# Kernel optimization log

Measured on AMD Instinct MI355X. Metric: run time of the kernel, lower is better.

Reference implementation:

```python
import jax, jax.numpy as jnp
import numpy as np

IN_CH, OUT_CH, HEADS = 256, 128, 4
DIM_HEAD = OUT_CH // HEADS  # 32 (module overrides dim_head = out_ch // heads)
R = 16  # reduce_size
EPS = 1e-5


def _conv3d(x, w, groups=1, pad=0):
    return jax.lax.conv_general_dilated(
        x, w, (1, 1, 1), [(pad, pad)] * 3,
        dimension_numbers=('NCDHW', 'OIDHW', 'NCDHW'),
        feature_group_count=groups)


def _dwsep(x, wd, wp):
    # depthwise 3x3x3 (groups=C) then pointwise 1x1x1, both bias-free
    y = _conv3d(x, wd, groups=x.shape[1], pad=1)
    return _conv3d(y, wp)


def _bn(x, g, b):
    # training-mode BatchNorm3d: biased batch stats over (N, D, H, W)
    m = x.mean(axis=(0, 2, 3, 4), keepdims=True)
    v = x.var(axis=(0, 2, 3, 4), keepdims=True)
    return (x - m) * jax.lax.rsqrt(v + EPS) * g.reshape(1, -1, 1, 1, 1) + b.reshape(1, -1, 1, 1, 1)


def _interp1(x, axis, out_len):
    in_len = x.shape[axis]
    if in_len == out_len:
        return x
    pos = jnp.arange(out_len, dtype=x.dtype) * ((in_len - 1) / (out_len - 1))  # align_corners=True
    lo = jnp.clip(jnp.floor(pos).astype(jnp.int32), 0, in_len - 1)
    hi = jnp.clip(lo + 1, 0, in_len - 1)
    w = pos - lo.astype(x.dtype)
    shp = [1] * x.ndim
    shp[axis] = out_len
    w = w.reshape(shp)
    return jnp.take(x, lo, axis=axis) * (1 - w) + jnp.take(x, hi, axis=axis) * w


def _interp3(x, size):
    for ax, s in zip((2, 3, 4), size):
        x = _interp1(x, ax, s)
    return x


def _rel_index(h, w, d):
    c = np.stack(np.meshgrid(np.arange(h), np.arange(w), np.arange(d), indexing='ij')).reshape(3, -1)
    rel = (c[:, :, None] - c[:, None, :]).transpose(1, 2, 0).astype(np.int64)
    rel[:, :, 0] += h - 1
    rel[:, :, 1] += w - 1
    rel[:, :, 0] *= 2 * h - 1
    idx = rel.sum(-1)
    # faithful to torch: negative indices wrap around the table
    return idx % ((2 * h - 1) * (2 * w - 1) * (2 * d - 1))


def _rel_bias(table, h, w, d, H, W, D, heads):
    idx = _rel_index(h, w, d)
    bias = table[idx.reshape(-1)].reshape(h, w, d, h * w, -1)
    bias = jnp.repeat(bias, H // h, axis=0)
    bias = jnp.repeat(bias, W // w, axis=1)
    bias = jnp.repeat(bias, D // d, axis=2)
    return bias.reshape(H * W * D, h * w * d, heads).transpose(2, 0, 1)[None]  # [1,heads,Nq,Nk]


def setup_inputs() -> dict:
    key = jax.random.key(0)
    ks = jax.random.split(key, 12)
    n = lambda k, s: jax.random.normal(k, s, dtype=jnp.float32)
    return {
        'x1': n(ks[0], (1, IN_CH, 8, 8, 8)),
        'x2': n(ks[1], (1, OUT_CH, 16, 16, 16)),
        'w_ch': n(ks[2], (OUT_CH, IN_CH, 1, 1, 1)) * 0.05,
        'b_ch': jnp.zeros((OUT_CH,), jnp.float32),
        'gamma_l': jnp.ones((IN_CH,), jnp.float32), 'beta_l': jnp.zeros((IN_CH,), jnp.float32),
        'gamma_h': jnp.ones((OUT_CH,), jnp.float32), 'beta_h': jnp.zeros((OUT_CH,), jnp.float32),
        'gamma2': jnp.ones((OUT_CH,), jnp.float32), 'beta2': jnp.zeros((OUT_CH,), jnp.float32),
        'kv_dw': n(ks[3], (IN_CH, 1, 3, 3, 3)) * 0.05,
        'kv_pw': n(ks[4], (2 * OUT_CH, IN_CH, 1, 1, 1)) * 0.05,
        'q_dw': n(ks[5], (OUT_CH, 1, 3, 3, 3)) * 0.05,
        'q_pw': n(ks[6], (OUT_CH, OUT_CH, 1, 1, 1)) * 0.05,
        'out_dw': n(ks[7], (OUT_CH, 1, 3, 3, 3)) * 0.05,
        'out_pw': n(ks[8], (OUT_CH, OUT_CH, 1, 1, 1)) * 0.05,
        'w_mlp': n(ks[9], (OUT_CH, OUT_CH, 1, 1, 1)) * 0.05,
        'rel_table': n(ks[10], ((2 * R - 1) ** 3, HEADS)) * 0.02,
    }


def reference(x1, x2, w_ch, b_ch, gamma_l, beta_l, gamma_h, beta_h, gamma2, beta2,
              kv_dw, kv_pw, q_dw, q_pw, out_dw, out_pw, w_mlp, rel_table):
    B, C, H, W, D = x1.shape
    _, _, HH, WH, DH = x2.shape
    residue = _interp3(_conv3d(x1, w_ch) + b_ch.reshape(1, -1, 1, 1, 1), (HH, WH, DH))
    x1n = _bn(x1, gamma_l, beta_l)
    x2n = _bn(x2, gamma_h, beta_h)
    k, v = jnp.split(_dwsep(x1n, kv_dw, kv_pw), 2, axis=1)
    q = _dwsep(x2n, q_dw, q_pw)
    if H != R:
        k = _interp3(k, (R, R, R))
        v = _interp3(v, (R, R, R))

    def heads_split(t, h, w_, d):
        # channel layout is (dim_head, heads)
        t = t.reshape(B, DIM_HEAD, HEADS, h, w_, d)
        return t.transpose(0, 2, 3, 4, 5, 1).reshape(B, HEADS, h * w_ * d, DIM_HEAD)

    qh = heads_split(q, HH, WH, DH)
    kh = heads_split(k, R, R, R)
    vh = heads_split(v, R, R, R)
    attn = jnp.einsum('bhid,bhjd->bhij', qh, kh)
    attn = attn + _rel_bias(rel_table, R, R, R, HH, WH, DH, HEADS)
    attn = jax.nn.softmax(attn * (DIM_HEAD ** -0.5), axis=-1)  # note: bias is scaled too, as in source
    o = jnp.einsum('bhij,bhjd->bhid', attn, vh)
    o = o.reshape(B, HEADS, HH, WH, DH, DIM_HEAD).transpose(0, 5, 1, 2, 3, 4).reshape(B, OUT_CH, HH, WH, DH)
    o = _dwsep(o, out_dw, out_pw)
    o = o + residue
    res2 = o
    o = jax.nn.relu(_bn(o, gamma2, beta2))
    o = _conv3d(o, w_mlp)
    return o + res2
```

## Files before the change

kernel.cpp:

```cpp
#include <hip/hip_runtime.h>
#include <hip/hip_bf16.h>

using f32x4  = __attribute__((ext_vector_type(4))) float;
using bf16x8 = __attribute__((ext_vector_type(8))) short;
using i32x4  = __attribute__((ext_vector_type(4))) int;

static constexpr float SCALE = 0.17677669529663687f;
static constexpr float L2E   = 1.4426950408889634f;
static constexpr float SL    = SCALE * L2E;

__device__ inline int cvtpk(float lo, float hi) {
  int r;
  asm("v_cvt_pk_bf16_f32 %0,%1,%2" : "=v"(r) : "v"(lo), "v"(hi));
  return r;
}

__device__ inline void bred2(float& s, float& ss) {
  #pragma unroll
  for (int off = 32; off; off >>= 1) {
    s  += __shfl_down(s, off, 64);
    ss += __shfl_down(ss, off, 64);
  }
  __shared__ float as_[4], ass_[4];
  int wid = threadIdx.x >> 6;
  if ((threadIdx.x & 63) == 0) { as_[wid] = s; ass_[wid] = ss; }
  __syncthreads();
  s  = as_[0] + as_[1] + as_[2] + as_[3];
  ss = ass_[0] + ass_[1] + ass_[2] + ass_[3];
}

__global__ __launch_bounds__(256) void bnstat_both_kernel(
    const float* __restrict__ x1, const float* __restrict__ x2,
    const float* __restrict__ gl, const float* __restrict__ bl,
    const float* __restrict__ gh, const float* __restrict__ bh,
    float* __restrict__ ab_l, float* __restrict__ ab_h) {
  int b = blockIdx.x;
  const float* src; const float *gamma, *beta; float* ab; int S, C, c;
  if (b < 256) { c = b;       src = x1 + (size_t)c * 512;  S = 512;  C = 256; gamma = gl; beta = bl; ab = ab_l; }
  else         { c = b - 256; src = x2 + (size_t)c * 4096; S = 4096; C = 128; gamma = gh; beta = bh; ab = ab_h; }
  float s = 0.f, ss = 0.f;
  for (int i = threadIdx.x; i < S; i += 256) { float v = src[i]; s += v; ss = fmaf(v, v, ss); }
  bred2(s, ss);
  if (threadIdx.x == 0) {
    float inv = 1.0f / (float)S;
    float m   = s * inv;
    float var = ss * inv - m * m;
    float a   = gamma[c] * rsqrtf(var + 1e-5f);
    ab[c]     = a;
    ab[C + c] = beta[c] - m * a;
  }
}

template<bool AFF>
__device__ inline void dw_body(
    const float* __restrict__ in, const float* __restrict__ w,
    const float* __restrict__ ab, float* __restrict__ out,
    int n, int nn, int n3, int C, int t) {
  int c = t / n3, s = t - c * n3;
  int z = s / nn, r = s - z * nn, y = r / n, x = r - y * n;
  const float* src = in + (size_t)c * n3;
  const float* wc  = w + c * 27;
  float a = 1.f, b = 0.f;
  if (AFF) { a = ab[c]; b = ab[C + c]; }
  float acc = 0.f;
  #pragma unroll
  for (int kd = 0; kd < 3; kd++) {
    int zz = z + kd - 1;
    if (zz < 0 || zz >= n) continue;
    #pragma unroll
    for (int kh = 0; kh < 3; kh++) {
      int yy = y + kh - 1;
      if (yy < 0 || yy >= n) continue;
      #pragma unroll
      for (int kw = 0; kw < 3; kw++) {
        int xx = x + kw - 1;
        if (xx < 0 || xx >= n) continue;
        float v = src[(zz * n + yy) * n + xx];
        if (AFF) v = fmaf(v, a, b);
        acc = fmaf(v, wc[kd * 9 + kh * 3 + kw], acc);
      }
    }
  }
  out[t] = acc;
}

__global__ __launch_bounds__(256) void stageA_kernel(
    const float* __restrict__ x1, const float* __restrict__ x2,
    const float* __restrict__ w_ch, const float* __restrict__ b_ch,
    const float* __restrict__ kv_dw, const float* __restrict__ q_dw,
    const float* __restrict__ ab_l, const float* __restrict__ ab_h,
    float* __restrict__ res8, float* __restrict__ kvdw, float* __restrict__ qdw) {
  int b = blockIdx.x;
  if (b < 128) {
    int oc0 = (b >> 1) * 2;
    int s   = (b & 1) * 256 + threadIdx.x;
    float a0 = 0.f, a1 = 0.f;
    const float* w0 = w_ch + (size_t)oc0 * 256;
    const float* w1 = w0 + 256;
    #pragma unroll 8
    for (int ic = 0; ic < 256; ic++) {
      float x = x1[(size_t)ic * 512 + s];
      a0 = fmaf(w0[ic], x, a0);
      a1 = fmaf(w1[ic], x, a1);
    }
    res8[(size_t)oc0 * 512 + s]       = a0 + b_ch[oc0];
    res8[(size_t)(oc0 + 1) * 512 + s] = a1 + b_ch[oc0 + 1];
  } else if (b < 640) {
    dw_body<true>(x1, kv_dw, ab_l, kvdw, 8, 64, 512, 256, (b - 128) * 256 + threadIdx.x);
  } else {
    dw_body<true>(x2, q_dw, ab_h, qdw, 16, 256, 4096, 128, (b - 640) * 256 + threadIdx.x);
  }
}

__device__ inline void icoef8(int o, int& lo, int& hi, float& w) {
  float p = (float)o * (7.0f / 15.0f);
  int l = (int)floorf(p);
  if (l > 7) l = 7;
  int h = l + 1 > 7 ? 7 : l + 1;
  w  = p - (float)l;
  lo = l; hi = h;
}

__device__ inline float trilin8(const float* __restrict__ p,
                                int z0, int z1, float wz,
                                int y0, int y1, float wy,
                                int x0, int x1, float wx) {
  float c00 = p[(z0*8+y0)*8+x0]*(1.f-wx) + p[(z0*8+y0)*8+x1]*wx;
  float c01 = p[(z0*8+y1)*8+x0]*(1.f-wx) + p[(z0*8+y1)*8+x1]*wx;
  float c10 = p[(z1*8+y0)*8+x0]*(1.f-wx) + p[(z1*8+y0)*8+x1]*wx;
  float c11 = p[(z1*8+y1)*8+x0]*(1.f-wx) + p[(z1*8+y1)*8+x1]*wx;
  float c0 = c00*(1.f-wy) + c01*wy;
  float c1 = c10*(1.f-wy) + c11*wy;
  return c0*(1.f-wz) + c1*wz;
}

__global__ __launch_bounds__(512) void stageB_kernel(
    const float* __restrict__ kvdw, const float* __restrict__ kv_pw,
    const float* __restrict__ qdw, const float* __restrict__ q_pw,
    const float* __restrict__ res8,
    unsigned short* __restrict__ Kb, unsigned short* __restrict__ Vt,
    unsigned short* __restrict__ Qpk, float* __restrict__ r16) {
  __shared__ float sm[2][512];
  int b = blockIdx.x;
  int tid = threadIdx.x;
  if (b < 128) {
    int kc0 = b * 2;
    int s = tid;
    float a0 = 0.f, a1 = 0.f;
    const float* w0 = kv_pw + (size_t)kc0 * 256;
    const float* w1 = w0 + 256;
    #pragma unroll 8
    for (int ic = 0; ic < 256; ic++) {
      float x = kvdw[(size_t)ic * 512 + s];
      a0 = fmaf(w0[ic], x, a0);
      a1 = fmaf(w1[ic], x, a1);
    }
    sm[0][s] = a0; sm[1][s] = a1;
    __syncthreads();
    #pragma unroll
    for (int r = 0; r < 16; r++) {
      int u  = r * 512 + tid;
      int cl = u >> 12, j = u & 4095;
      int z = j >> 8, y = (j >> 4) & 15, x = j & 15;
      int z0,z1,y0,y1,x0,x1; float wz,wy,wx;
      icoef8(z, z0, z1, wz); icoef8(y, y0, y1, wy); icoef8(x, x0, x1, wx);
      float val = trilin8(sm[cl], z0, z1, wz, y0, y1, wy, x0, x1, wx);
      __hip_bfloat16 bv = __float2bfloat16(val);
      unsigned short us = *reinterpret_cast<unsigned short*>(&bv);
      int kc = kc0 + cl;
      int c  = kc & 127;
      int head = c & 3, dh = c >> 2;
      if (kc < 128) Kb[((size_t)(head << 12) + j) * 32 + dh] = us;
      else          Vt[((size_t)(head * 32) + dh) * 4096 + j] = us;
    }
  } else if (b < 256) {
    int bb   = b - 128;
    int head = bb >> 5;
    int r2   = bb & 31;
    int dh0  = (r2 >> 3) * 8;
    int i    = (r2 & 7) * 512 + tid;
    float acc[8];
    #pragma unroll
    for (int e = 0; e < 8; e++) acc[e] = 0.f;
    #pragma unroll 4
    for (int ic = 0; ic < 128; ic++) {
      float x = qdw[(size_t)ic * 4096 + i];
      #pragma unroll
      for (int e = 0; e < 8; e++)
        acc[e] = fmaf(q_pw[(size_t)((dh0 + e) * 4 + head) * 128 + ic], x, acc[e]);
    }
    i32x4 pk = { cvtpk(acc[0], acc[1]), cvtpk(acc[2], acc[3]),
                 cvtpk(acc[4], acc[5]), cvtpk(acc[6], acc[7]) };
    *reinterpret_cast<i32x4*>(Qpk + ((size_t)(head << 12) + i) * 32 + dh0) = pk;
  } else {
    int t = (b - 256) * 512 + tid;
    int s = t & 4095, c = t >> 12;
    int z = s >> 8, y = (s >> 4) & 15, x = s & 15;
    int z0,z1,y0,y1,x0,x1; float wz,wy,wx;
    icoef8(z, z0, z1, wz); icoef8(y, y0, y1, wy); icoef8(x, x0, x1, wx);
    r16[t] = trilin8(res8 + c * 512, z0, z1, wz, y0, y1, wy, x0, x1, wx);
  }
}

__global__ __launch_bounds__(512, 4) void attn_mfma_kernel(
    const unsigned short* __restrict__ Qpk, const unsigned short* __restrict__ Kb,
    const unsigned short* __restrict__ Vt, const float* __restrict__ table,
    float* __restrict__ o_sp) {
  __shared__ float lut[992];
  __shared__ float red_o[8 * 64 * 9];
  __shared__ float red_ml[2][8][16];
  int head  = blockIdx.x >> 8;
  int strip = blockIdx.x & 255;
  for (int u = threadIdx.x; u < 991; u += 512) {
    int p = (u < 15) ? (u - 15 + 29791) : (u - 15);
    lut[u] = table[p * 4 + head] * SL;
  }
  __syncthreads();

  int w    = threadIdx.x >> 6;
  int lane = threadIdx.x & 63;
  int qrow = lane & 15;
  int g    = lane >> 4;
  int i    = strip * 16 + qrow;
  int iz = i >> 8, iy = (i >> 4) & 15, ix = i & 15;
  int lanebase = iz * 31 + iy + ix;

  bf16x8 qf = *(const bf16x8*)(Qpk + ((size_t)(head << 12) + i) * 32 + g * 8);

  const unsigned short* Kh = Kb + (size_t)head * 4096 * 32;
  const unsigned short* Vh = Vt + (size_t)head * 32 * 4096;

  f32x4 zero = {0.f, 0.f, 0.f, 0.f};
  f32x4 accO0 = zero, accO1 = zero;
  float m2 = -1e30f, lpart = 0.f;

  int kt0 = w * 16;
  bf16x8 kf0 = *(const bf16x8*)(Kh + ((size_t)(kt0 * 32 + qrow)) * 32 + g * 8);
  bf16x8 kf1 = *(const bf16x8*)(Kh + ((size_t)(kt0 * 32 + 16 + qrow)) * 32 + g * 8);
  bf16x8 vf0 = *(const bf16x8*)(Vh + (size_t)(qrow)  * 4096 + kt0 * 32 + g * 8);
  bf16x8 vf1 = *(const bf16x8*)(Vh + (size_t)(16 + qrow) * 4096 + kt0 * 32 + g * 8);

  for (int ktl = 0; ktl < 16; ktl++) {
    int kt  = kt0 + ktl;
    int nkt = kt0 + ((ktl + 1) & 15);
    bf16x8 nk0 = *(const bf16x8*)(Kh + ((size_t)(nkt * 32 + qrow)) * 32 + g * 8);
    bf16x8 nk1 = *(const bf16x8*)(Kh + ((size_t)(nkt * 32 + 16 + qrow)) * 32 + g * 8);
    bf16x8 nv0 = *(const bf16x8*)(Vh + (size_t)(qrow)  * 4096 + nkt * 32 + g * 8);
    bf16x8 nv1 = *(const bf16x8*)(Vh + (size_t)(16 + qrow) * 4096 + nkt * 32 + g * 8);

    f32x4 accA = __builtin_amdgcn_mfma_f32_16x16x32_bf16(kf0, qf, zero, 0, 0, 0);
    f32x4 accB = __builtin_amdgcn_mfma_f32_16x16x32_bf16(kf1, qf, zero, 0, 0, 0);

    int z0 = kt >> 3, y0 = (kt << 1) & 15;
    int Cc = 495 - 31 * z0 - y0;
    const float* lp = &lut[lanebase + Cc - 4 * g - 4];
    float l0 = lp[0], l1 = lp[1], l2 = lp[2], l3 = lp[3], l4 = lp[4];

    float t0 = fmaf(accA[0], SL, l4);
    float t1 = fmaf(accA[1], SL, l3);
    float t2 = fmaf(accA[2], SL, l2);
    float t3 = fmaf(accA[3], SL, l1);
    float t4 = fmaf(accB[0], SL, l3);
    float t5 = fmaf(accB[1], SL, l2);
    float t6 = fmaf(accB[2], SL, l1);
    float t7 = fmaf(accB[3], SL, l0);

    float cm = fmaxf(fmaxf(fmaxf(t0, t1), fmaxf(t2, t3)),
                     fmaxf(fmaxf(t4, t5), fmaxf(t6, t7)));
    cm = fmaxf(cm, __shfl_xor(cm, 16, 64));
    cm = fmaxf(cm, __shfl_xor(cm, 32, 64));

    if (__any(cm > m2 + 8.f)) {
      float mn   = fmaxf(m2, cm);
      float corr = exp2f(m2 - mn);
      m2 = mn;
      lpart *= corr;
      accO0[0] *= corr; accO0[1] *= corr; accO0[2] *= corr; accO0[3] *= corr;
      accO1[0] *= corr; accO1[1] *= corr; accO1[2] *= corr; accO1[3] *= corr;
    }

    float p0 = exp2f(t0 - m2), p1 = exp2f(t1 - m2);
    float p2 = exp2f(t2 - m2), p3 = exp2f(t3 - m2);
    float p4 = exp2f(t4 - m2), p5 = exp2f(t5 - m2);
    float p6 = exp2f(t6 - m2), p7 = exp2f(t7 - m2);
    lpart += ((p0 + p1) + (p2 + p3)) + ((p4 + p5) + (p6 + p7));

    int w0 = cvtpk(p0, p1), w1 = cvtpk(p2, p3);
    int w2 = cvtpk(p4, p5), w3 = cvtpk(p6, p7);
    int srcA = ((g & 1) << 5) + qrow;
    int srcB = srcA + 16;
    int x0 = __shfl(w0, srcA, 64), x1 = __shfl(w1, srcA, 64);
    int x2 = __shfl(w2, srcA, 64), x3 = __shfl(w3, srcA, 64);
    int y0s = __shfl(w0, srcB, 64), y1s = __shfl(w1, srcB, 64);
    int y2s = __shfl(w2, srcB, 64), y3s = __shfl(w3, srcB, 64);
    bool thi = (g >> 1) != 0;
    union { i32x4 i4; bf16x8 s8; } up;
    up.i4 = (i32x4){ thi ? x2 : x0, thi ? x3 : x1,
                     thi ? y2s : y0s, thi ? y3s : y1s };

    accO0 = __builtin_amdgcn_mfma_f32_16x16x32_bf16(vf0, up.s8, accO0, 0, 0, 0);
    accO1 = __builtin_amdgcn_mfma_f32_16x16x32_bf16(vf1, up.s8, accO1, 0, 0, 0);

    kf0 = nk0; kf1 = nk1; vf0 = nv0; vf1 = nv1;
  }

  float lsum = lpart + __shfl_xor(lpart, 16, 64);
  lsum += __shfl_xor(lsum, 32, 64);

  int lbase = (w * 64 + lane) * 9;
  #pragma unroll
  for (int r = 0; r < 4; r++) { red_o[lbase + r] = accO0[r]; red_o[lbase + 4 + r] = accO1[r]; }
  if (g == 0) { red_ml[0][w][qrow] = m2; red_ml[1][w][qrow] = lsum; }
  __syncthreads();

  if (w == 0) {
    float ml[8];
    float mx = -1e30f;
    #pragma unroll
    for (int wv = 0; wv < 8; wv++) { ml[wv] = red_ml[0][wv][qrow]; mx = fmaxf(mx, ml[wv]); }
    float c[8];
    float L = 0.f;
    #pragma unroll
    for (int wv = 0; wv < 8; wv++) {
      c[wv] = exp2f(ml[wv] - mx);
      L = fmaf(c[wv], red_ml[1][wv][qrow], L);
    }
    float inv = 1.0f / L;
    #pragma unroll
    for (int r = 0; r < 8; r++) {
      float o = 0.f;
      #pragma unroll
      for (int wv = 0; wv < 8; wv++)
        o = fmaf(c[wv], red_o[(wv * 64 + lane) * 9 + r], o);
      int d0 = (r < 4) ? (4 * g + r) : (16 + 4 * g + (r - 4));
      o_sp[(size_t)(d0 * 4 + head) * 4096 + i] = o * inv;
    }
  }
}

__global__ __launch_bounds__(256) void dw_out_kernel(
    const float* __restrict__ in, const float* __restrict__ w, float* __restrict__ out) {
  dw_body<false>(in, w, nullptr, out, 16, 256, 4096, 128, blockIdx.x * 256 + threadIdx.x);
}

__global__ __launch_bounds__(256) void pw_out_kernel(
    const float* __restrict__ in, const float* __restrict__ w,
    const float* __restrict__ r16, float* __restrict__ res2,
    float* __restrict__ sums) {
  __shared__ float red[4][2][2];
  int oc0 = (blockIdx.x >> 3) * 2;
  int sb  = blockIdx.x & 7;
  int s0  = (sb * 256 + threadIdx.x) * 2;
  float a00 = 0.f, a01 = 0.f, a10 = 0.f, a11 = 0.f;
  const float* w0 = w + (size_t)oc0 * 128;
  const float* w1 = w0 + 128;
  #pragma unroll 8
  for (int ic = 0; ic < 128; ic++) {
    float xa = in[(size_t)ic * 4096 + s0];
    float xb = in[(size_t)ic * 4096 + s0 + 1];
    float wv0 = w0[ic], wv1 = w1[ic];
    a00 = fmaf(wv0, xa, a00); a01 = fmaf(wv0, xb, a01);
    a10 = fmaf(wv1, xa, a10); a11 = fmaf(wv1, xb, a11);
  }
  size_t ob0 = (size_t)oc0 * 4096 + s0;
  size_t ob1 = ob0 + 4096;
  float r00 = a00 + r16[ob0],     r01 = a01 + r16[ob0 + 1];
  float r10 = a10 + r16[ob1],     r11 = a11 + r16[ob1 + 1];
  res2[ob0] = r00; res2[ob0 + 1] = r01;
  res2[ob1] = r10; res2[ob1 + 1] = r11;
  float s_0 = r00 + r01, q_0 = fmaf(r00, r00, r01 * r01);
  float s_1 = r10 + r11, q_1 = fmaf(r10, r10, r11 * r11);
  #pragma unroll
  for (int off = 32; off; off >>= 1) {
    s_0 += __shfl_down(s_0, off, 64); q_0 += __shfl_down(q_0, off, 64);
    s_1 += __shfl_down(s_1, off, 64); q_1 += __shfl_down(q_1, off, 64);
  }
  int wid = threadIdx.x >> 6;
  if ((threadIdx.x & 63) == 0) {
    red[wid][0][0] = s_0; red[wid][0][1] = q_0;
    red[wid][1][0] = s_1; red[wid][1][1] = q_1;
  }
  __syncthreads();
  if (threadIdx.x < 2) {
    int o = threadIdx.x;
    float st = red[0][o][0] + red[1][o][0] + red[2][o][0] + red[3][o][0];
    float qt = red[0][o][1] + red[1][o][1] + red[2][o][1] + red[3][o][1];
    sums[(oc0 + o) * 8 + sb]        = st;
    sums[1024 + (oc0 + o) * 8 + sb] = qt;
  }
}

__global__ __launch_bounds__(256) void pw_mlp_kernel(
    const float* __restrict__ res2, const float* __restrict__ w,
    const float* __restrict__ gamma2, const float* __restrict__ beta2,
    const float* __restrict__ sums, float* __restrict__ out) {
  __shared__ float A[128], Bb[128];
  if (threadIdx.x < 128) {
    int c = threadIdx.x;
    float s = 0.f, q = 0.f;
    #pragma unroll
    for (int sb = 0; sb < 8; sb++) { s += sums[c * 8 + sb]; q += sums[1024 + c * 8 + sb]; }
    float m   = s * (1.0f / 4096.0f);
    float var = q * (1.0f / 4096.0f) - m * m;
    float a   = gamma2[c] * rsqrtf(var + 1e-5f);
    A[c]  = a;
    Bb[c] = beta2[c] - m * a;
  }
  __syncthreads();
  int oc0 = (blockIdx.x >> 3) * 2;
  int sb  = blockIdx.x & 7;
  int s0  = (sb * 256 + threadIdx.x) * 2;
  float a00 = 0.f, a01 = 0.f, a10 = 0.f, a11 = 0.f;
  const float* w0 = w + (size_t)oc0 * 128;
  const float* w1 = w0 + 128;
  #pragma unroll 8
  for (int ic = 0; ic < 128; ic++) {
    float aa = A[ic], bb = Bb[ic];
    float xa = fmaxf(fmaf(res2[(size_t)ic * 4096 + s0], aa, bb), 0.f);
    float xb = fmaxf(fmaf(res2[(size_t)ic * 4096 + s0 + 1], aa, bb), 0.f);
    float wv0 = w0[ic], wv1 = w1[ic];
    a00 = fmaf(wv0, xa, a00); a01 = fmaf(wv0, xb, a01);
    a10 = fmaf(wv1, xa, a10); a11 = fmaf(wv1, xb, a11);
  }
  size_t ob0 = (size_t)oc0 * 4096 + s0;
  size_t ob1 = ob0 + 4096;
  out[ob0]     = a00 + res2[ob0];
  out[ob0 + 1] = a01 + res2[ob0 + 1];
  out[ob1]     = a10 + res2[ob1];
  out[ob1 + 1] = a11 + res2[ob1 + 1];
}

extern "C" void kernel_launch(void* const* d_in, const int* in_sizes, int n_in,
                              void* d_out, int out_size, void* d_ws, size_t ws_size,
                              hipStream_t stream) {
  (void)in_sizes; (void)n_in; (void)out_size; (void)ws_size;
  const float* x1      = (const float*)d_in[0];
  const float* x2      = (const float*)d_in[1];
  const float* w_ch    = (const float*)d_in[2];
  const float* b_ch    = (const float*)d_in[3];
  const float* gamma_l = (const float*)d_in[4];
  const float* beta_l  = (const float*)d_in[5];
  const float* gamma_h = (const float*)d_in[6];
  const float* beta_h  = (const float*)d_in[7];
  const float* gamma2  = (const float*)d_in[8];
  const float* beta2   = (const float*)d_in[9];
  const float* kv_dw   = (const float*)d_in[10];
  const float* kv_pw   = (const float*)d_in[11];
  const float* q_dw    = (const float*)d_in[12];
  const float* q_pw    = (const float*)d_in[13];
  const float* out_dw  = (const float*)d_in[14];
  const float* out_pw  = (const float*)d_in[15];
  const float* w_mlp   = (const float*)d_in[16];
  const float* rtab    = (const float*)d_in[17];

  float* ws = (float*)d_ws;
  float* ab_l = ws + 0;
  float* ab_h = ws + 512;
  float* sums = ws + 768;
  float* res8 = ws + 2816;
  float* kvdw = ws + 68352;
  float* qdw  = ws + 199424;
  unsigned short* Qpk = (unsigned short*)(ws + 723712);
  unsigned short* Kb  = (unsigned short*)(ws + 985856);
  unsigned short* Vt  = (unsigned short*)(ws + 1248000);
  float* r16  = ws + 1510144;
  float* o_sp = ws + 2034432;
  float* odw  = ws + 2558720;
  float* res2 = ws + 3083008;

  bnstat_both_kernel<<<384, 256, 0, stream>>>(x1, x2, gamma_l, beta_l, gamma_h, beta_h,
                                              ab_l, ab_h);
  stageA_kernel<<<2688, 256, 0, stream>>>(x1, x2, w_ch, b_ch, kv_dw, q_dw,
                                          ab_l, ab_h, res8, kvdw, qdw);
  stageB_kernel<<<1280, 512, 0, stream>>>(kvdw, kv_pw, qdw, q_pw, res8,
                                          Kb, Vt, Qpk, r16);
  attn_mfma_kernel<<<1024, 512, 0, stream>>>(Qpk, Kb, Vt, rtab, o_sp);
  dw_out_kernel<<<2048, 256, 0, stream>>>(o_sp, out_dw, odw);
  pw_out_kernel<<<512, 256, 0, stream>>>(odw, out_pw, r16, res2, sums);
  pw_mlp_kernel<<<512, 256, 0, stream>>>(res2, w_mlp, gamma2, beta2, sums, (float*)d_out);
}
```

Before: 122.2 us.

## Share K/V tiles across waves via LDS and split keys across blocks

```diff
diff --git a/kernel.cpp b/kernel.cpp
--- a/kernel.cpp
+++ b/kernel.cpp
@@ -205,23 +205,26 @@
 __global__ __launch_bounds__(512, 4) void attn_mfma_kernel(
     const unsigned short* __restrict__ Qpk, const unsigned short* __restrict__ Kb,
     const unsigned short* __restrict__ Vt, const float* __restrict__ table,
-    float* __restrict__ o_sp) {
+    float* __restrict__ part_o, float* __restrict__ part_m, float* __restrict__ part_l) {
   __shared__ float lut[992];
-  __shared__ float red_o[8 * 64 * 9];
-  __shared__ float red_ml[2][8][16];
-  int head  = blockIdx.x >> 8;
-  int strip = blockIdx.x & 255;
-  for (int u = threadIdx.x; u < 991; u += 512) {
+  __shared__ unsigned short kvs[2][4096];
+
+  int head = blockIdx.x >> 8;
+  int rem  = blockIdx.x & 255;
+  int qg   = rem >> 3;
+  int ksb  = rem & 7;
+  int tid  = threadIdx.x;
+
+  for (int u = tid; u < 991; u += 512) {
     int p = (u < 15) ? (u - 15 + 29791) : (u - 15);
     lut[u] = table[p * 4 + head] * SL;
   }
-  __syncthreads();
-
-  int w    = threadIdx.x >> 6;
-  int lane = threadIdx.x & 63;
+
+  int w    = tid >> 6;
+  int lane = tid & 63;
   int qrow = lane & 15;
   int g    = lane >> 4;
-  int i    = strip * 16 + qrow;
+  int i    = qg * 128 + w * 16 + qrow;
   int iz = i >> 8, iy = (i >> 4) & 15, ix = i & 15;
   int lanebase = iz * 31 + iy + ix;
 
@@ -229,24 +232,51 @@
 
   const unsigned short* Kh = Kb + (size_t)head * 4096 * 32;
   const unsigned short* Vh = Vt + (size_t)head * 32 * 4096;
+
+  int kt0 = ksb * 16;
+
+  const unsigned short* src;
+  size_t sstride;
+  if (tid < 256) {
+    int key = tid >> 2, s = tid & 3;
+    int gp  = s ^ ((key >> 1) & 3);
+    src = Kh + (size_t)(kt0 * 32 + key) * 32 + gp * 8;
+    sstride = 32 * 32;
+  } else {
+    int tt = tid - 256;
+    int dh = tt >> 2, s = tt & 3;
+    int gp = s ^ ((dh >> 1) & 3);
+    src = Vh + (size_t)dh * 4096 + kt0 * 32 + gp * 8;
+    sstride = 32;
+  }
+  int t8 = tid * 8;
+
+  int sw    = (qrow >> 1) & 3;
+  int k0off = qrow * 32 + ((g ^ sw) * 8);
+  int k1off = k0off + 512;
+  int v0off = 2048 + k0off;
+  int v1off = v0off + 512;
+
+  {
+    bf16x8 s0 = *(const bf16x8*)src; src += sstride;
+    *(bf16x8*)(&kvs[0][t8]) = s0;
+  }
+  __syncthreads();
 
   f32x4 zero = {0.f, 0.f, 0.f, 0.f};
   f32x4 accO0 = zero, accO1 = zero;
   float m2 = -1e30f, lpart = 0.f;
-
-  int kt0 = w * 16;
-  bf16x8 kf0 = *(const bf16x8*)(Kh + ((size_t)(kt0 * 32 + qrow)) * 32 + g * 8);
-  bf16x8 kf1 = *(const bf16x8*)(Kh + ((size_t)(kt0 * 32 + 16 + qrow)) * 32 + g * 8);
-  bf16x8 vf0 = *(const bf16x8*)(Vh + (size_t)(qrow)  * 4096 + kt0 * 32 + g * 8);
-  bf16x8 vf1 = *(const bf16x8*)(Vh + (size_t)(16 + qrow) * 4096 + kt0 * 32 + g * 8);
+  int cur = 0;
 
   for (int ktl = 0; ktl < 16; ktl++) {
-    int kt  = kt0 + ktl;
-    int nkt = kt0 + ((ktl + 1) & 15);
-    bf16x8 nk0 = *(const bf16x8*)(Kh + ((size_t)(nkt * 32 + qrow)) * 32 + g * 8);
-    bf16x8 nk1 = *(const bf16x8*)(Kh + ((size_t)(nkt * 32 + 16 + qrow)) * 32 + g * 8);
-    bf16x8 nv0 = *(const bf16x8*)(Vh + (size_t)(qrow)  * 4096 + nkt * 32 + g * 8);
-    bf16x8 nv1 = *(const bf16x8*)(Vh + (size_t)(16 + qrow) * 4096 + nkt * 32 + g * 8);
+    int kt = kt0 + ktl;
+    bf16x8 stg;
+    if (ktl < 15) { stg = *(const bf16x8*)src; src += sstride; }
+
+    bf16x8 kf0 = *(const bf16x8*)(&kvs[cur][k0off]);
+    bf16x8 kf1 = *(const bf16x8*)(&kvs[cur][k1off]);
+    bf16x8 vf0 = *(const bf16x8*)(&kvs[cur][v0off]);
+    bf16x8 vf1 = *(const bf16x8*)(&kvs[cur][v1off]);
 
     f32x4 accA = __builtin_amdgcn_mfma_f32_16x16x32_bf16(kf0, qf, zero, 0, 0, 0);
     f32x4 accB = __builtin_amdgcn_mfma_f32_16x16x32_bf16(kf1, qf, zero, 0, 0, 0);
@@ -301,40 +331,48 @@
     accO0 = __builtin_amdgcn_mfma_f32_16x16x32_bf16(vf0, up.s8, accO0, 0, 0, 0);
     accO1 = __builtin_amdgcn_mfma_f32_16x16x32_bf16(vf1, up.s8, accO1, 0, 0, 0);
 
-    kf0 = nk0; kf1 = nk1; vf0 = nv0; vf1 = nv1;
+    if (ktl < 15) *(bf16x8*)(&kvs[cur ^ 1][t8]) = stg;
+    __syncthreads();
+    cur ^= 1;
   }
 
   float lsum = lpart + __shfl_xor(lpart, 16, 64);
   lsum += __shfl_xor(lsum, 32, 64);
 
-  int lbase = (w * 64 + lane) * 9;
-  #pragma unroll
-  for (int r = 0; r < 4; r++) { red_o[lbase + r] = accO0[r]; red_o[lbase + 4 + r] = accO1[r]; }
-  if (g == 0) { red_ml[0][w][qrow] = m2; red_ml[1][w][qrow] = lsum; }
-  __syncthreads();
-
-  if (w == 0) {
-    float ml[8];
-    float mx = -1e30f;
+  int base = head * 8 + ksb;
+  if (g == 0) {
+    part_m[base * 4096 + i] = m2;
+    part_l[base * 4096 + i] = lsum;
+  }
+  #pragma unroll
+  for (int r = 0; r < 4; r++) {
+    part_o[(size_t)(base * 32 + 4 * g + r) * 4096 + i]      = accO0[r];
+    part_o[(size_t)(base * 32 + 16 + 4 * g + r) * 4096 + i] = accO1[r];
+  }
+}
+
+__global__ __launch_bounds__(256) void attn_reduce_kernel(
+    const float* __restrict__ part_o, const float* __restrict__ part_m,
+    const float* __restrict__ part_l, float* __restrict__ o_sp) {
+  int t = blockIdx.x * 256 + threadIdx.x;
+  int i = t & 4095, head = t >> 12;
+  float mk[8], mx = -1e30f;
+  #pragma unroll
+  for (int ks = 0; ks < 8; ks++) { mk[ks] = part_m[(head*8+ks)*4096 + i]; mx = fmaxf(mx, mk[ks]); }
+  float c[8], L = 0.f;
+  #pragma unroll
+  for (int ks = 0; ks < 8; ks++) {
+    c[ks] = exp2f(mk[ks] - mx);
+    L = fmaf(c[ks], part_l[(head*8+ks)*4096 + i], L);
+  }
+  float invL = 1.f / L;
+  #pragma unroll
+  for (int d = 0; d < 32; d++) {
+    float acc = 0.f;
     #pragma unroll
-    for (int wv = 0; wv < 8; wv++) { ml[wv] = red_ml[0][wv][qrow]; mx = fmaxf(mx, ml[wv]); }
-    float c[8];
-    float L = 0.f;
-    #pragma unroll
-    for (int wv = 0; wv < 8; wv++) {
-      c[wv] = exp2f(ml[wv] - mx);
-      L = fmaf(c[wv], red_ml[1][wv][qrow], L);
-    }
-    float inv = 1.0f / L;
-    #pragma unroll
-    for (int r = 0; r < 8; r++) {
-      float o = 0.f;
-      #pragma unroll
-      for (int wv = 0; wv < 8; wv++)
-        o = fmaf(c[wv], red_o[(wv * 64 + lane) * 9 + r], o);
-      int d0 = (r < 4) ? (4 * g + r) : (16 + 4 * g + (r - 4));
-      o_sp[(size_t)(d0 * 4 + head) * 4096 + i] = o * inv;
-    }
+    for (int ks = 0; ks < 8; ks++)
+      acc = fmaf(c[ks], part_o[(size_t)((head*8+ks)*32 + d) * 4096 + i], acc);
+    o_sp[(size_t)(d * 4 + head) * 4096 + i] = acc * invL;
   }
 }
 
@@ -467,6 +505,9 @@
   float* o_sp = ws + 2034432;
   float* odw  = ws + 2558720;
   float* res2 = ws + 3083008;
+  float* part_o = ws + 3607296;
+  float* part_m = ws + 7801600;
+  float* part_l = ws + 7932672;
 
   bnstat_both_kernel<<<384, 256, 0, stream>>>(x1, x2, gamma_l, beta_l, gamma_h, beta_h,
                                               ab_l, ab_h);
@@ -474,7 +515,9 @@
                                           ab_l, ab_h, res8, kvdw, qdw);
   stageB_kernel<<<1280, 512, 0, stream>>>(kvdw, kv_pw, qdw, q_pw, res8,
                                           Kb, Vt, Qpk, r16);
-  attn_mfma_kernel<<<1024, 512, 0, stream>>>(Qpk, Kb, Vt, rtab, o_sp);
+  attn_mfma_kernel<<<1024, 512, 0, stream>>>(Qpk, Kb, Vt, rtab,
+                                             part_o, part_m, part_l);
+  attn_reduce_kernel<<<64, 256, 0, stream>>>(part_o, part_m, part_l, o_sp);
   dw_out_kernel<<<2048, 256, 0, stream>>>(o_sp, out_dw, odw);
   pw_out_kernel<<<512, 256, 0, stream>>>(odw, out_pw, r16, res2, sums);
   pw_mlp_kernel<<<512, 256, 0, stream>>>(res2, w_mlp, gamma2, beta2, sums, (float*)d_out);
```

Measured after the change: 112.5 us. -8.0%, faster.
